# Performance work log

Hardware: AMD Instinct MI355X
Metric: run time of the kernel (lower is better)

Reference implementation:

```python
import jax, jax.numpy as jnp
import numpy as np

B, S, D = 2, 2048, 1024
H = 16
HD = D // H  # head_dim = 64


def _xavier(key, shape):
    fan_out, fan_in = shape
    bound = jnp.sqrt(6.0 / (fan_in + fan_out))
    return jax.random.uniform(key, shape, jnp.float32, -bound, bound)


def setup_inputs() -> dict:
    key = jax.random.key(0)
    kx, kqkv, ko = jax.random.split(key, 3)
    x = jax.random.normal(kx, (B, S, D), jnp.float32)
    # torch nn.Linear stores weight as [out, in]; we keep that layout and use x @ W.T
    W_qkv = _xavier(kqkv, (3 * D, D))
    b_qkv = jnp.zeros((3 * D,), jnp.float32)
    W_o = _xavier(ko, (D, D))
    b_o = jnp.zeros((D,), jnp.float32)
    return {"x": x, "W_qkv": W_qkv, "b_qkv": b_qkv, "W_o": W_o, "b_o": b_o}


def reference(x, W_qkv, b_qkv, W_o, b_o):
    b, s, d = x.shape
    h, hd = H, HD
    # qkv projection: [b, s, 3d]
    qkv = jnp.einsum("bsd,ed->bse", x, W_qkv) + b_qkv
    # [b, s, h, 3*hd] -> [b, h, s, 3*hd]
    qkv = qkv.reshape(b, s, h, 3 * hd).transpose(0, 2, 1, 3)
    q, k, v = jnp.split(qkv, 3, axis=-1)
    scale = 1.0 / jnp.sqrt(jnp.asarray(hd, x.dtype))
    logits = jnp.einsum("bhqd,bhkd->bhqk", q, k) * scale
    attn = jax.nn.softmax(logits, axis=-1)
    values = jnp.einsum("bhqk,bhkd->bhqd", attn, v)
    values = values.transpose(0, 2, 1, 3).reshape(b, s, d)
    return jnp.einsum("bsd,ed->bse", values, W_o) + b_o
```

## Files before the change

### kernel.cpp

```cpp
#include <hip/hip_runtime.h>

typedef unsigned short u16;
typedef __attribute__((ext_vector_type(8))) short bf16x8;
typedef __attribute__((ext_vector_type(4))) float f32x4;
typedef __attribute__((ext_vector_type(16))) float f32x16;
typedef __attribute__((ext_vector_type(4))) unsigned short u16x4;

__device__ __forceinline__ u16 f2bf(float f) {
    unsigned u = __float_as_uint(f);
    u = u + 0x7FFFu + ((u >> 16) & 1u);
    return (u16)(u >> 16);
}

__device__ __forceinline__ void gload16(const void* g, void* l) {
    __builtin_amdgcn_global_load_lds(
        (const __attribute__((address_space(1))) unsigned int*)g,
        (__attribute__((address_space(3))) unsigned int*)l,
        16, 0, 0);
}

__device__ __forceinline__ f32x4 mfma16(bf16x8 a, bf16x8 b, f32x4 c) {
    return __builtin_amdgcn_mfma_f32_16x16x32_bf16(a, b, c, 0, 0, 0);
}
__device__ __forceinline__ f32x16 mfma32(bf16x8 a, bf16x8 b, f32x16 c) {
    return __builtin_amdgcn_mfma_f32_32x32x16_bf16(a, b, c, 0, 0, 0);
}

__global__ __launch_bounds__(256) void cvt_all(const float* __restrict__ x,
                                               const float* __restrict__ wqkv,
                                               const float* __restrict__ wo,
                                               u16* __restrict__ dst) {
    int i = blockIdx.x * 256 + threadIdx.x;
    float4 v;
    if (i < 1048576)       v = ((const float4*)x)[i];
    else if (i < 1835008)  v = ((const float4*)wqkv)[i - 1048576];
    else                   v = ((const float4*)wo)[i - 1835008];
    u16x4 o = { f2bf(v.x), f2bf(v.y), f2bf(v.z), f2bf(v.w) };
    ((u16x4*)dst)[i] = o;
}

template <int BM, int BN, bool OUT_BF16>
__global__ __launch_bounds__(256) void gemm_bt(const u16* __restrict__ A,
                                               const u16* __restrict__ Bm,
                                               const float* __restrict__ bias,
                                               void* __restrict__ Cp,
                                               int M, int N, int K) {
    constexpr int FM = BM / 32, FN = BN / 32;
    __shared__ u16 As[2][BM * 64];
    __shared__ u16 Bs[2][BN * 64];
    const int tid = threadIdx.x, lane = tid & 63, wave = tid >> 6;
    const int wr = wave >> 1, wc = wave & 1;
    const int l15 = lane & 15, l4 = lane >> 4;

    const int nx = gridDim.x, nwg = nx * gridDim.y;
    const int id = blockIdx.y * nx + blockIdx.x;
    const int wg = (id & 7) * (nwg >> 3) + (id >> 3);
    const int m0 = (wg / nx) * BM, n0 = (wg % nx) * BN;

    f32x4 zero = {0.f, 0.f, 0.f, 0.f};
    f32x4 acc[FM][FN];
#pragma unroll
    for (int m = 0; m < FM; ++m)
#pragma unroll
        for (int n = 0; n < FN; ++n) acc[m][n] = zero;

#define STAGE_BT(tt, buf) {                                                 \
    _Pragma("unroll")                                                       \
    for (int i = 0; i < BM / 32; ++i) {                                     \
        int c = i * 256 + tid;                                              \
        int r = c >> 3, kc = (c & 7) ^ (r & 7);                             \
        gload16(A + (size_t)(m0 + r) * K + (tt) * 64 + kc * 8,              \
                &As[buf][(i * 256 + wave * 64) * 8]);                       \
    }                                                                       \
    _Pragma("unroll")                                                       \
    for (int i = 0; i < BN / 32; ++i) {                                     \
        int c = i * 256 + tid;                                              \
        int r = c >> 3, kc = (c & 7) ^ (r & 7);                             \
        gload16(Bm + (size_t)(n0 + r) * K + (tt) * 64 + kc * 8,             \
                &Bs[buf][(i * 256 + wave * 64) * 8]);                       \
    } }

    const int nt = K >> 6;
    STAGE_BT(0, 0);
    for (int t = 0; t < nt; ++t) {
        asm volatile("s_waitcnt vmcnt(0)" ::: "memory");
        asm volatile("s_barrier" ::: "memory");
        if (t < nt - 1) { STAGE_BT(t + 1, (t + 1) & 1); }
        const char* Asb = (const char*)As[t & 1];
        const char* Bsb = (const char*)Bs[t & 1];
#pragma unroll
        for (int kk = 0; kk < 2; ++kk) {
            bf16x8 af[FM], bfr[FN];
#pragma unroll
            for (int m = 0; m < FM; ++m) {
                int row = wr * (BM / 2) + m * 16 + l15;
                int ch = (kk * 4 + l4) ^ (row & 7);
                af[m] = *(const bf16x8*)(Asb + row * 128 + ch * 16);
            }
#pragma unroll
            for (int n = 0; n < FN; ++n) {
                int row = wc * (BN / 2) + n * 16 + l15;
                int ch = (kk * 4 + l4) ^ (row & 7);
                bfr[n] = *(const bf16x8*)(Bsb + row * 128 + ch * 16);
            }
#pragma unroll
            for (int m = 0; m < FM; ++m)
#pragma unroll
                for (int n = 0; n < FN; ++n)
                    acc[m][n] = mfma16(af[m], bfr[n], acc[m][n]);
        }
    }
#undef STAGE_BT
    float bv[FN];
#pragma unroll
    for (int n = 0; n < FN; ++n) bv[n] = bias[n0 + wc * (BN / 2) + n * 16 + l15];
#pragma unroll
    for (int m = 0; m < FM; ++m) {
#pragma unroll
        for (int j = 0; j < 4; ++j) {
            size_t row = (size_t)(m0 + wr * (BM / 2) + m * 16 + l4 * 4 + j);
#pragma unroll
            for (int n = 0; n < FN; ++n) {
                int col = n0 + wc * (BN / 2) + n * 16 + l15;
                float v = acc[m][n][j] + bv[n];
                if (OUT_BF16)
                    ((u16*)Cp)[row * (size_t)N + col] = f2bf(v);
                else
                    ((float*)Cp)[row * (size_t)N + col] = v;
            }
        }
    }
}

__global__ __launch_bounds__(512) void gemm256(const u16* __restrict__ A,
                                               const u16* __restrict__ Bm,
                                               const float* __restrict__ bias,
                                               u16* __restrict__ Cp,
                                               u16* __restrict__ Vt,
                                               int M, int N, int K) {
    __shared__ __align__(16) char lds[131072];
    const int tid = threadIdx.x, lane = tid & 63, wave = tid >> 6;
    const int wr = wave >> 2, wc = wave & 3;
    const int l15 = lane & 15, l4 = lane >> 4;

    const int nx = gridDim.x, nwg = nx * gridDim.y;
    const int id = blockIdx.y * nx + blockIdx.x;
    const int wg = (id & 7) * (nwg >> 3) + (id >> 3);
    const int m0 = (wg / nx) * 256, n0 = (wg % nx) * 256;

    const u16* asrc[2][2];
    const u16* bsrc[2][2];
#pragma unroll
    for (int q = 0; q < 2; ++q)
#pragma unroll
        for (int r = 0; r < 2; ++r) {
            int c = r * 512 + tid;
            int lr = c >> 3;
            int kc = (c & 7) ^ (lr & 7);
            asrc[q][r] = A  + (size_t)(m0 + lr + (lr & 64) + q * 64) * K + kc * 8;
            bsrc[q][r] = Bm + (size_t)(n0 + lr + (lr & 96) + q * 32) * K + kc * 8;
        }
    const int sd0 = wave * 1024;
    const int sd1 = 8192 + wave * 1024;

    const int roA = (wr * 64 + l15) * 128;
    const int roB = (wc * 32 + l15) * 128;
    int ch16[2];
#pragma unroll
    for (int kk = 0; kk < 2; ++kk) ch16[kk] = ((kk * 4 + l4) ^ (l15 & 7)) * 16;

    f32x4 zero = {0.f, 0.f, 0.f, 0.f};
    f32x4 acc[2][2][4][2];
#pragma unroll
    for (int a = 0; a < 2; ++a)
#pragma unroll
        for (int b = 0; b < 2; ++b)
#pragma unroll
            for (int c = 0; c < 4; ++c)
#pragma unroll
                for (int d = 0; d < 2; ++d) acc[a][b][c][d] = zero;

#define STG_A(q, tt) { char* rb = lds + (((tt) & 1) * 32768) + (q) * 16384;          \
        gload16(asrc[q][0] + (size_t)(tt) * 64, rb + sd0);                            \
        gload16(asrc[q][1] + (size_t)(tt) * 64, rb + sd1); }
#define STG_B(q, tt) { char* rb = lds + 65536 + (((tt) & 1) * 32768) + (q) * 16384;  \
        gload16(bsrc[q][0] + (size_t)(tt) * 64, rb + sd0);                            \
        gload16(bsrc[q][1] + (size_t)(tt) * 64, rb + sd1); }
#define MFMA_PH(MH, NH) {                                                             \
        __builtin_amdgcn_s_setprio(1);                                                \
        _Pragma("unroll")                                                             \
        for (int fm = 0; fm < 4; ++fm)                                                \
            _Pragma("unroll")                                                         \
            for (int fn = 0; fn < 2; ++fn)                                            \
                _Pragma("unroll")                                                     \
                for (int kk = 0; kk < 2; ++kk)                                        \
                    acc[MH][NH][fm][fn] =                                             \
                        mfma16(af[fm][kk], bfr[NH][fn][kk], acc[MH][NH][fm][fn]);     \
        __builtin_amdgcn_s_setprio(0); }

    STG_A(0, 0); STG_B(0, 0); STG_A(1, 0); STG_B(1, 0);
    asm volatile("s_waitcnt vmcnt(4)" ::: "memory");
    asm volatile("s_barrier" ::: "memory");

    bf16x8 af[4][2], bfr[2][2][2];
    const int nt = K >> 6;
    for (int t = 0; t < nt; ++t) {
        const char* Ab = lds + (t & 1) * 32768;
        const char* Bb = lds + 65536 + (t & 1) * 32768;
#pragma unroll
        for (int fm = 0; fm < 4; ++fm)
#pragma unroll
            for (int kk = 0; kk < 2; ++kk)
                af[fm][kk] = *(const bf16x8*)(Ab + roA + fm * 2048 + ch16[kk]);
#pragma unroll
        for (int fn = 0; fn < 2; ++fn)
#pragma unroll
            for (int kk = 0; kk < 2; ++kk)
                bfr[0][fn][kk] = *(const bf16x8*)(Bb + roB + fn * 2048 + ch16[kk]);
        if (t < nt - 1) STG_A(0, t + 1);
        asm volatile("s_barrier" ::: "memory");
        MFMA_PH(0, 0);
        asm volatile("s_barrier" ::: "memory");
#pragma unroll
        for (int fn = 0; fn < 2; ++fn)
#pragma unroll
            for (int kk = 0; kk < 2; ++kk)
                bfr[1][fn][kk] = *(const bf16x8*)(Bb + 16384 + roB + fn * 2048 + ch16[kk]);
        if (t < nt - 1) STG_B(0, t + 1);
        asm volatile("s_barrier" ::: "memory");
        MFMA_PH(0, 1);
        if (t < nt - 1) asm volatile("s_waitcnt vmcnt(4)" ::: "memory");
        else            asm volatile("s_waitcnt vmcnt(0)" ::: "memory");
        asm volatile("s_barrier" ::: "memory");
#pragma unroll
        for (int fm = 0; fm < 4; ++fm)
#pragma unroll
            for (int kk = 0; kk < 2; ++kk)
                af[fm][kk] = *(const bf16x8*)(Ab + 16384 + roA + fm * 2048 + ch16[kk]);
        if (t < nt - 1) STG_A(1, t + 1);
        asm volatile("s_barrier" ::: "memory");
        MFMA_PH(1, 0);
        asm volatile("s_barrier" ::: "memory");
        if (t < nt - 1) STG_B(1, t + 1);
        asm volatile("s_barrier" ::: "memory");
        MFMA_PH(1, 1);
        if (t < nt - 1) asm volatile("s_waitcnt vmcnt(4)" ::: "memory");
        asm volatile("s_barrier" ::: "memory");
    }
#undef STG_A
#undef STG_B
#undef MFMA_PH

    float bv[2][2];
#pragma unroll
    for (int nh = 0; nh < 2; ++nh)
#pragma unroll
        for (int fn = 0; fn < 2; ++fn)
            bv[nh][fn] = bias[n0 + wc * 64 + nh * 32 + fn * 16 + l15];
#pragma unroll
    for (int mh = 0; mh < 2; ++mh)
#pragma unroll
        for (int fm = 0; fm < 4; ++fm)
#pragma unroll
            for (int j = 0; j < 4; ++j) {
                size_t row = (size_t)(m0 + wr * 128 + mh * 64 + fm * 16 + l4 * 4 + j);
#pragma unroll
                for (int nh = 0; nh < 2; ++nh)
#pragma unroll
                    for (int fn = 0; fn < 2; ++fn) {
                        int col = n0 + wc * 64 + nh * 32 + fn * 16 + l15;
                        Cp[row * (size_t)N + col] =
                            f2bf(acc[mh][nh][fm][fn][j] + bv[nh][fn]);
                    }
            }

    const int b_ = m0 >> 11, s0_ = m0 & 2047;
    const int hmin = (n0 + 63) / 192;
    const int nV = ((hmin + 1) * 192 + 128 < n0 + 256) ? 128 : 64;
#pragma unroll
    for (int nh = 0; nh < 2; ++nh)
#pragma unroll
        for (int fn = 0; fn < 2; ++fn) {
            int col = n0 + wc * 64 + nh * 32 + fn * 16 + l15;
            int hh = col / 192;
            int dd = col - hh * 192 - 128;
            if (dd >= 0) {
                int vl = (hh - hmin) * 64 + dd;
#pragma unroll
                for (int mh = 0; mh < 2; ++mh)
#pragma unroll
                    for (int fm = 0; fm < 4; ++fm) {
                        int r0 = wr * 128 + mh * 64 + fm * 16 + l4 * 4;
                        u16x4 w = { f2bf(acc[mh][nh][fm][fn][0] + bv[nh][fn]),
                                    f2bf(acc[mh][nh][fm][fn][1] + bv[nh][fn]),
                                    f2bf(acc[mh][nh][fm][fn][2] + bv[nh][fn]),
                                    f2bf(acc[mh][nh][fm][fn][3] + bv[nh][fn]) };
                        *(u16x4*)(lds + vl * 520 + r0 * 2) = w;
                    }
            }
        }
    __syncthreads();
    {
        size_t vt_base = ((size_t)(b_ * 16 + hmin) * 64) * 2048 + s0_;
        int nchunks = nV * 64;
        for (int c = tid; c < nchunks; c += 512) {
            int vl = c >> 6, sl = c & 63;
            u16x4 w = *(const u16x4*)(lds + vl * 520 + sl * 8);
            *(u16x4*)(Vt + (size_t)vl * 2048 + vt_base + sl * 4) = w;
        }
    }
}

__global__ __launch_bounds__(512, 4) void attn_kernel(const u16* __restrict__ qkv,
                                                      const u16* __restrict__ Vt,
                                                      u16* __restrict__ vals) {
    __shared__ __align__(16) char lds[65536];
    const int L = blockIdx.x;
    const int ord = L >> 3;
    const int hb = (L & 7) * 4 + (ord >> 4);
    const int qt = ord & 15;
    const int h = hb & 15, b = hb >> 4;
    const int tid = threadIdx.x, lane = tid & 63, wave = tid >> 6;
    const int gtid = tid & 255, qsub = wave & 3, kvh = wave >> 2;
    const int l31 = lane & 31, hi = lane >> 5;
    const float S2E = 0.18033688f;

    const u16* qbase = qkv + (size_t)(b * 2048 + qt * 128 + qsub * 32 + l31) * 3072 + h * 192;
    bf16x8 Qf[4];
#pragma unroll
    for (int ks = 0; ks < 4; ++ks) {
        bf16x8 q = *(const bf16x8*)(qbase + ks * 16 + hi * 8);
#pragma unroll
        for (int j = 0; j < 8; ++j) {
            float f = __uint_as_float(((unsigned)(u16)q[j]) << 16) * S2E;
            q[j] = (short)f2bf(f);
        }
        Qf[ks] = q;
    }

    bf16x8 ones;
#pragma unroll
    for (int j = 0; j < 8; ++j) ones[j] = (short)0x3F80;

    const u16* kp[2];
    const u16* vp[2];
    int dst[2];
#pragma unroll
    for (int i = 0; i < 2; ++i) {
        int c = i * 256 + gtid;
        int fi = c >> 6, dl = c & 63;
        int mm = fi >> 2, ks = fi & 3;
        int row = mm * 32 + (dl & 31);
        int col = ks * 16 + (dl >> 5) * 8;
        kp[i] = qkv + (size_t)(b * 2048 + kvh * 1024 + row) * 3072 + h * 192 + 64 + col;
        vp[i] = Vt + ((size_t)((b * 16 + h) * 64 + row)) * 2048 + kvh * 1024 + col;
        dst[i] = fi * 512;
    }
    u16* Kst = (u16*)lds + kvh * 8192;
    u16* Vst = (u16*)lds + 16384 + kvh * 8192;

    f32x16 accO[2], accL;
#pragma unroll
    for (int md = 0; md < 2; ++md)
#pragma unroll
        for (int r = 0; r < 16; ++r) accO[md][r] = 0.f;
#pragma unroll
    for (int r = 0; r < 16; ++r) accL[r] = 0.f;

    const char* KsL = (const char*)Kst + lane * 16;
    const char* VsL = (const char*)Vst + lane * 16;

#pragma unroll
    for (int i = 0; i < 2; ++i) gload16(kp[i], Kst + dst[i]);
#pragma unroll
    for (int i = 0; i < 2; ++i) gload16(vp[i], Vst + dst[i]);
#pragma unroll
    for (int i = 0; i < 2; ++i) { kp[i] += 64 * 3072; vp[i] += 64; }

    for (int t = 0; t < 16; ++t) {
        asm volatile("s_waitcnt vmcnt(0)" ::: "memory");
        asm volatile("s_barrier" ::: "memory");

        if (t < 15) {
            u16* kd = Kst + ((t + 1) & 1) * 4096;
            u16* vd = Vst + ((t + 1) & 1) * 4096;
#pragma unroll
            for (int i = 0; i < 2; ++i) gload16(kp[i], kd + dst[i]);
#pragma unroll
            for (int i = 0; i < 2; ++i) gload16(vp[i], vd + dst[i]);
#pragma unroll
            for (int i = 0; i < 2; ++i) { kp[i] += 64 * 3072; vp[i] += 64; }
        }

        const char* Kb = KsL + (t & 1) * 8192;
        const char* Vb = VsL + (t & 1) * 8192;

        f32x16 sc[2];
        __builtin_amdgcn_s_setprio(1);
#pragma unroll
        for (int m = 0; m < 2; ++m) {
            f32x16 c;
#pragma unroll
            for (int r = 0; r < 16; ++r) c[r] = 0.f;
#pragma unroll
            for (int ks = 0; ks < 4; ++ks) {
                bf16x8 kf = *(const bf16x8*)(Kb + (m * 4 + ks) * 1024);
                c = mfma32(kf, Qf[ks], c);
            }
            sc[m] = c;
        }
        __builtin_amdgcn_s_setprio(0);

        bf16x8 Pf[4];
#pragma unroll
        for (int r = 0; r < 16; ++r)
            sc[0][r] = __builtin_amdgcn_exp2f(sc[0][r]);
        {
            unsigned W0[4], W1[4];
#pragma unroll
            for (int g = 0; g < 4; ++g) {
                asm("v_cvt_pk_bf16_f32 %0, %1, %2"
                    : "=v"(W0[g]) : "v"(sc[0][4 * g + 0]), "v"(sc[0][4 * g + 1]));
                asm("v_cvt_pk_bf16_f32 %0, %1, %2"
                    : "=v"(W1[g]) : "v"(sc[0][4 * g + 2]), "v"(sc[0][4 * g + 3]));
            }
#pragma unroll
            for (int kpair = 0; kpair < 2; ++kpair) {
                unsigned xa = W0[2 * kpair], ya = W0[2 * kpair + 1];
                unsigned xb = W1[2 * kpair], yb = W1[2 * kpair + 1];
                asm volatile("v_permlane32_swap_b32 %0, %1" : "+v"(xa), "+v"(ya));
                asm volatile("v_permlane32_swap_b32 %0, %1" : "+v"(xb), "+v"(yb));
                union { unsigned w[4]; bf16x8 v; } u;
                u.w[0] = xa; u.w[1] = xb; u.w[2] = ya; u.w[3] = yb;
                Pf[kpair] = u.v;
            }
        }

        __builtin_amdgcn_s_setprio(1);
#pragma unroll
        for (int md = 0; md < 2; ++md) {
            f32x16 c = accO[md];
#pragma unroll
            for (int ks = 0; ks < 2; ++ks) {
                bf16x8 vf = *(const bf16x8*)(Vb + (md * 4 + ks) * 1024);
                c = mfma32(vf, Pf[ks], c);
            }
            accO[md] = c;
        }
#pragma unroll
        for (int ks = 0; ks < 2; ++ks)
            accL = mfma32(ones, Pf[ks], accL);
        __builtin_amdgcn_s_setprio(0);

#pragma unroll
        for (int r = 0; r < 16; ++r)
            sc[1][r] = __builtin_amdgcn_exp2f(sc[1][r]);
        {
            unsigned W0[4], W1[4];
#pragma unroll
            for (int g = 0; g < 4; ++g) {
                asm("v_cvt_pk_bf16_f32 %0, %1, %2"
                    : "=v"(W0[g]) : "v"(sc[1][4 * g + 0]), "v"(sc[1][4 * g + 1]));
                asm("v_cvt_pk_bf16_f32 %0, %1, %2"
                    : "=v"(W1[g]) : "v"(sc[1][4 * g + 2]), "v"(sc[1][4 * g + 3]));
            }
#pragma unroll
            for (int kpair = 0; kpair < 2; ++kpair) {
                unsigned xa = W0[2 * kpair], ya = W0[2 * kpair + 1];
                unsigned xb = W1[2 * kpair], yb = W1[2 * kpair + 1];
                asm volatile("v_permlane32_swap_b32 %0, %1" : "+v"(xa), "+v"(ya));
                asm volatile("v_permlane32_swap_b32 %0, %1" : "+v"(xb), "+v"(yb));
                union { unsigned w[4]; bf16x8 v; } u;
                u.w[0] = xa; u.w[1] = xb; u.w[2] = ya; u.w[3] = yb;
                Pf[2 + kpair] = u.v;
            }
        }

        __builtin_amdgcn_s_setprio(1);
#pragma unroll
        for (int md = 0; md < 2; ++md) {
            f32x16 c = accO[md];
#pragma unroll
            for (int ks = 2; ks < 4; ++ks) {
                bf16x8 vf = *(const bf16x8*)(Vb + (md * 4 + ks) * 1024);
                c = mfma32(vf, Pf[ks], c);
            }
            accO[md] = c;
        }
#pragma unroll
        for (int ks = 2; ks < 4; ++ks)
            accL = mfma32(ones, Pf[ks], accL);
        __builtin_amdgcn_s_setprio(0);
    }

    float lt = accL[0];

    float* MO = (float*)lds;
    float* ML = (float*)(lds + 32768);
    __syncthreads();
    if (kvh == 1) {
        int r = qsub * 64 + lane;
#pragma unroll
        for (int md = 0; md < 2; ++md)
#pragma unroll
            for (int g = 0; g < 4; ++g)
#pragma unroll
                for (int j = 0; j < 4; ++j)
                    MO[(md * 16 + 4 * g + j) * 256 + r] = accO[md][4 * g + j];
        ML[r] = lt;
    }
    __syncthreads();
    if (kvh == 0) {
        int r = qsub * 64 + lane;
        float inv = 1.f / (lt + ML[r]);
        size_t rowoff = (size_t)(b * 2048 + qt * 128 + qsub * 32 + l31) * 1024 + h * 64;
#pragma unroll
        for (int md = 0; md < 2; ++md)
#pragma unroll
            for (int g = 0; g < 4; ++g) {
                float w0 = MO[(md * 16 + 4 * g + 0) * 256 + r];
                float w1 = MO[(md * 16 + 4 * g + 1) * 256 + r];
                float w2 = MO[(md * 16 + 4 * g + 2) * 256 + r];
                float w3 = MO[(md * 16 + 4 * g + 3) * 256 + r];
                u16x4 o = { f2bf((accO[md][4 * g + 0] + w0) * inv),
                            f2bf((accO[md][4 * g + 1] + w1) * inv),
                            f2bf((accO[md][4 * g + 2] + w2) * inv),
                            f2bf((accO[md][4 * g + 3] + w3) * inv) };
                *(u16x4*)(vals + rowoff + md * 32 + 8 * g + 4 * hi) = o;
            }
    }
}

extern "C" void kernel_launch(void* const* d_in, const int* in_sizes, int n_in,
                              void* d_out, int out_size, void* d_ws, size_t ws_size,
                              hipStream_t stream) {
    const float* x    = (const float*)d_in[0];
    const float* Wqkv = (const float*)d_in[1];
    const float* bqkv = (const float*)d_in[2];
    const float* Wo   = (const float*)d_in[3];
    const float* bo   = (const float*)d_in[4];
    float* out = (float*)d_out;

    char* ws = (char*)d_ws;
    u16* x_bf    = (u16*)(ws);
    u16* Wqkv_bf = (u16*)(ws + 8388608);
    u16* Wo_bf   = (u16*)(ws + 14680064);
    u16* qkv_bf  = (u16*)(ws + 16777216);
    u16* Vt      = (u16*)(ws + 41943040);
    u16* vals    = (u16*)(ws + 50331648);

    cvt_all<<<8192, 256, 0, stream>>>(x, Wqkv, Wo, x_bf);

    gemm256<<<dim3(12, 16), 512, 0, stream>>>(x_bf, Wqkv_bf, bqkv, qkv_bf, Vt,
                                              4096, 3072, 1024);

    attn_kernel<<<512, 512, 0, stream>>>(qkv_bf, Vt, vals);

    gemm_bt<128, 64, false><<<dim3(16, 32), 256, 0, stream>>>(vals, Wo_bf, bo,
                                                              (void*)out, 4096, 1024, 1024);
}
```

Measured before the change: 112.4 us.

## Compute softmax row sums with VALU adds and stagger KV tile start order

Replaces the ones-vector MFMA used to accumulate softmax denominators with per-lane scalar sums of the exponentiated scores, combined across half-waves by a permlane32 swap at the end. This removes four MFMAs per iteration and a 16-register accumulator, at the cost of extra VALU adds, and the sums now use fp32 probabilities rather than bf16-rounded ones. It also rotates the starting KV tile for odd-ordered blocks by eight, so concurrent blocks read different K/V regions, aiming to spread memory traffic and reduce cache or channel contention.

```diff
diff --git a/kernel.cpp b/kernel.cpp
--- a/kernel.cpp
+++ b/kernel.cpp
@@ -320,6 +320,7 @@
     const int hb = (L & 7) * 4 + (ord >> 4);
     const int qt = ord & 15;
     const int h = hb & 15, b = hb >> 4;
+    const int st8 = (ord & 1) << 3;
     const int tid = threadIdx.x, lane = tid & 63, wave = tid >> 6;
     const int gtid = tid & 255, qsub = wave & 3, kvh = wave >> 2;
     const int l31 = lane & 31, hi = lane >> 5;
@@ -338,12 +339,8 @@
         Qf[ks] = q;
     }
 
-    bf16x8 ones;
-#pragma unroll
-    for (int j = 0; j < 8; ++j) ones[j] = (short)0x3F80;
-
-    const u16* kp[2];
-    const u16* vp[2];
+    const u16* kpb[2];
+    const u16* vpb[2];
     int dst[2];
 #pragma unroll
     for (int i = 0; i < 2; ++i) {
@@ -352,44 +349,40 @@
         int mm = fi >> 2, ks = fi & 3;
         int row = mm * 32 + (dl & 31);
         int col = ks * 16 + (dl >> 5) * 8;
-        kp[i] = qkv + (size_t)(b * 2048 + kvh * 1024 + row) * 3072 + h * 192 + 64 + col;
-        vp[i] = Vt + ((size_t)((b * 16 + h) * 64 + row)) * 2048 + kvh * 1024 + col;
+        kpb[i] = qkv + (size_t)(b * 2048 + kvh * 1024 + row) * 3072 + h * 192 + 64 + col;
+        vpb[i] = Vt + ((size_t)((b * 16 + h) * 64 + row)) * 2048 + kvh * 1024 + col;
         dst[i] = fi * 512;
     }
     u16* Kst = (u16*)lds + kvh * 8192;
     u16* Vst = (u16*)lds + 16384 + kvh * 8192;
 
-    f32x16 accO[2], accL;
+    f32x16 accO[2];
 #pragma unroll
     for (int md = 0; md < 2; ++md)
 #pragma unroll
         for (int r = 0; r < 16; ++r) accO[md][r] = 0.f;
-#pragma unroll
-    for (int r = 0; r < 16; ++r) accL[r] = 0.f;
+    float accLs = 0.f;
 
     const char* KsL = (const char*)Kst + lane * 16;
     const char* VsL = (const char*)Vst + lane * 16;
 
 #pragma unroll
-    for (int i = 0; i < 2; ++i) gload16(kp[i], Kst + dst[i]);
-#pragma unroll
-    for (int i = 0; i < 2; ++i) gload16(vp[i], Vst + dst[i]);
-#pragma unroll
-    for (int i = 0; i < 2; ++i) { kp[i] += 64 * 3072; vp[i] += 64; }
+    for (int i = 0; i < 2; ++i) gload16(kpb[i] + (size_t)st8 * 196608, Kst + dst[i]);
+#pragma unroll
+    for (int i = 0; i < 2; ++i) gload16(vpb[i] + (size_t)st8 * 64, Vst + dst[i]);
 
     for (int t = 0; t < 16; ++t) {
         asm volatile("s_waitcnt vmcnt(0)" ::: "memory");
         asm volatile("s_barrier" ::: "memory");
 
         if (t < 15) {
+            int phys = (t + 1 + st8) & 15;
             u16* kd = Kst + ((t + 1) & 1) * 4096;
             u16* vd = Vst + ((t + 1) & 1) * 4096;
 #pragma unroll
-            for (int i = 0; i < 2; ++i) gload16(kp[i], kd + dst[i]);
-#pragma unroll
-            for (int i = 0; i < 2; ++i) gload16(vp[i], vd + dst[i]);
-#pragma unroll
-            for (int i = 0; i < 2; ++i) { kp[i] += 64 * 3072; vp[i] += 64; }
+            for (int i = 0; i < 2; ++i) gload16(kpb[i] + (size_t)phys * 196608, kd + dst[i]);
+#pragma unroll
+            for (int i = 0; i < 2; ++i) gload16(vpb[i] + (size_t)phys * 64, vd + dst[i]);
         }
 
         const char* Kb = KsL + (t & 1) * 8192;
@@ -415,6 +408,13 @@
 #pragma unroll
         for (int r = 0; r < 16; ++r)
             sc[0][r] = __builtin_amdgcn_exp2f(sc[0][r]);
+        {
+            float q0 = (sc[0][0] + sc[0][1]) + (sc[0][2] + sc[0][3]);
+            float q1 = (sc[0][4] + sc[0][5]) + (sc[0][6] + sc[0][7]);
+            float q2 = (sc[0][8] + sc[0][9]) + (sc[0][10] + sc[0][11]);
+            float q3 = (sc[0][12] + sc[0][13]) + (sc[0][14] + sc[0][15]);
+            accLs += (q0 + q1) + (q2 + q3);
+        }
         {
             unsigned W0[4], W1[4];
 #pragma unroll
@@ -447,14 +447,18 @@
             }
             accO[md] = c;
         }
-#pragma unroll
-        for (int ks = 0; ks < 2; ++ks)
-            accL = mfma32(ones, Pf[ks], accL);
         __builtin_amdgcn_s_setprio(0);
 
 #pragma unroll
         for (int r = 0; r < 16; ++r)
             sc[1][r] = __builtin_amdgcn_exp2f(sc[1][r]);
+        {
+            float q0 = (sc[1][0] + sc[1][1]) + (sc[1][2] + sc[1][3]);
+            float q1 = (sc[1][4] + sc[1][5]) + (sc[1][6] + sc[1][7]);
+            float q2 = (sc[1][8] + sc[1][9]) + (sc[1][10] + sc[1][11]);
+            float q3 = (sc[1][12] + sc[1][13]) + (sc[1][14] + sc[1][15]);
+            accLs += (q0 + q1) + (q2 + q3);
+        }
         {
             unsigned W0[4], W1[4];
 #pragma unroll
@@ -487,13 +491,15 @@
             }
             accO[md] = c;
         }
-#pragma unroll
-        for (int ks = 2; ks < 4; ++ks)
-            accL = mfma32(ones, Pf[ks], accL);
         __builtin_amdgcn_s_setprio(0);
     }
 
-    float lt = accL[0];
+    float lt;
+    {
+        float xa = accLs, xb = accLs;
+        asm volatile("v_permlane32_swap_b32 %0, %1" : "+v"(xa), "+v"(xb));
+        lt = xa + xb;
+    }
 
     float* MO = (float*)lds;
     float* ML = (float*)(lds + 32768);
```

New measurement: 111.4 us. Within noise of the previous version (-0.8%).
